# Performance work log

Hardware: AMD Instinct MI355X
Metric: run time of the kernel (lower is better)

Reference implementation:

```python
import jax, jax.numpy as jnp
import numpy as np
import math

MU = 0.1
NU = 10.0
UNITS = [512] * 8
FEATURES = 1024
BATCH = 8192
EPS = 1e-5


def _norm(x):
    return jnp.linalg.norm(x) + EPS


def _cayley(W):
    # Cayley orthogonalization; matches the torch reference (recursive transpose for wide matrices).
    cout, cin = W.shape
    if cin > cout:
        return _cayley(W.T).T
    U, V = W[:cin], W[cin:]
    I = jnp.eye(cin, dtype=W.dtype)
    A = U - U.T + V.T @ V
    iIpA = jnp.linalg.inv(I + A)
    return jnp.concatenate([iIpA @ (I - A), -2.0 * V @ iIpA], axis=0)


def setup_inputs() -> dict:
    key = jax.random.key(0)
    ks = jax.random.split(key, 5)
    sum_units = sum(UNITS)
    # xavier-normal-ish scales
    x = jax.random.normal(ks[0], (BATCH, FEATURES), jnp.float32)
    Fq = jax.random.normal(ks[1], (sum_units, FEATURES), jnp.float32) * math.sqrt(2.0 / (sum_units + FEATURES))
    fq = _norm(Fq).reshape(1)  # init.constant_(fq, norm(Fq))
    by = jnp.zeros((FEATURES,), jnp.float32)
    nz = UNITS[0]
    Fr0 = jax.random.normal(ks[2], (nz, nz), jnp.float32) * math.sqrt(2.0 / (nz + nz))
    Fr_rest = jax.random.normal(ks[3], (len(UNITS) - 1, nz, 2 * nz), jnp.float32) * math.sqrt(2.0 / (nz + 2 * nz))
    fr0 = _norm(Fr0).reshape(1)
    fr_rest = jnp.linalg.norm(Fr_rest, axis=(1, 2)) + EPS
    fr = jnp.concatenate([fr0, fr_rest])
    b = jnp.zeros((len(UNITS), nz), jnp.float32)
    return {"x": x, "Fq": Fq, "fq": fq, "by": by, "Fr0": Fr0, "Fr_rest": Fr_rest, "fr": fr, "b": b}


def reference(x, Fq, fq, by, Fr0, Fr_rest, fr, b):
    sqrt_gam = math.sqrt(NU - MU)
    sqrt2 = math.sqrt(2.0)
    # per-forward Cayley orthogonalization (training path)
    Q = _cayley(fq[0] * Fq / _norm(Fq))  # (sum_units, features)
    Rs = [_cayley(fr[0] * Fr0 / _norm(Fr0))]
    for k in range(Fr_rest.shape[0]):
        Rs.append(_cayley(fr[k + 1] * Fr_rest[k] / _norm(Fr_rest[k])))

    xh = sqrt_gam * (x @ Q.T)  # (B, sum_units)
    yh = []
    hk_1 = xh[..., :0]  # empty start
    idx = 0
    for k, nz in enumerate(UNITS):
        xk = xh[..., idx:idx + nz]
        pre = sqrt2 * (jnp.concatenate([xk, hk_1], axis=-1) @ Rs[k].T) + b[k]
        gh = sqrt2 * (jax.nn.relu(pre) @ Rs[k])  # (B, nz + nz_prev)
        hk = gh[..., :nz] - xk
        gk = gh[..., nz:]
        yh.append(hk_1 - gk)
        idx += nz
        hk_1 = hk
    yh.append(hk_1)
    yh = jnp.concatenate(yh, axis=-1)  # (B, sum_units)
    return 0.5 * ((MU + NU) * x + sqrt_gam * (yh @ Q)) + by
```

## Files before the change

### kernel.cpp

```cpp
#include <hip/hip_runtime.h>
#include <math.h>


using s8v = __attribute__((ext_vector_type(8))) short;
using f4v = __attribute__((ext_vector_type(4))) float;
typedef unsigned short ush;
typedef unsigned int uint32;

#define DEV __device__ __forceinline__

DEV float b2f(ush u){ union{unsigned int i; float f;} v; v.i = ((unsigned int)u)<<16; return v.f; }
DEV ush f2b(float f){
  union{float f; unsigned int i;} v; v.f = f;
  unsigned int u = v.i;
  return (ush)((u + 0x7fffu + ((u>>16)&1u)) >> 16);
}

typedef __attribute__((address_space(1))) void gvoid;
typedef __attribute__((address_space(3))) void lvoid;
DEV void gload16(const void* g, void* l){
  __builtin_amdgcn_global_load_lds((gvoid*)g, (lvoid*)l, 16, 0, 0);
}

DEV void st16(ush* dst, const ush* a){
  *(int4*)dst = *(const int4*)a; *(int4*)(dst+8) = *(const int4*)(a+8);
}

struct GA {
  const ush *A0h, *A0l; long lda0;
  const ush *A1h, *A1l; long lda1; int ksplit;
  const ush *Bh, *Bl; long ldb;
  int K, M, N;
  float alpha, beta;
  long sA, sB, sO, sD;
  void *o0,*o1,*o2,*o3,*o4;
  const void *e0,*e1;
  long ldo0, ldo1, ldE;
};

enum { E_F32=0, E_BF16=1, E_BF16T2=2, E_SPLIT=3, E_QW=4, E_PRE=5, E_GH=6, E_OUT=7 };

template<int BM, int BN, int EPI, bool SPLIT, bool TRX>
__global__ __launch_bounds__(256) void gemm_k(GA gq, GA gr, int zsplit)
{
  constexpr int AH = BM*32;
  constexpr int BH = BN*32;
  constexpr int PANEL = (AH+BH) * (SPLIT ? 2 : 1);
  constexpr int TBN = TRX ? 64*65*2 : 0;
  constexpr int SMN = (3*PANEL > TBN) ? 3*PANEL : TBN;
  __shared__ ush smem[SMN] __attribute__((aligned(16)));
  uint32* tb = (uint32*)smem;

  constexpr int LPS = (BM/64 + BN/64) * (SPLIT ? 2 : 1);

  GA g; int bz;
  if ((int)blockIdx.z < zsplit){ g = gq; bz = blockIdx.z; }
  else                         { g = gr; bz = blockIdx.z - zsplit; }

  const int gx = gridDim.x, gy = gridDim.y;
  const int lin = blockIdx.y*gx + blockIdx.x;
  const int per = gx*8;
  const int grp = lin / per;
  const int rem = lin - grp*per;
  int gh = gy - grp*8; if (gh > 8) gh = 8;
  const int by = grp*8 + rem % gh;
  const int bx = rem / gh;
  const int m0 = by * BM;
  const int n0 = bx * BN;
  if (m0 >= g.M || n0 >= g.N) return;

  const int t = threadIdx.x;
  const int lane = t & 63;
  const int wave = t >> 6;
  const int wm = (wave >> 1) * (BM/2);
  const int wn = (wave & 1) * (BN/2);
  constexpr int MT = BM/32;
  constexpr int NT = BN/32;

  const ush* Ah  = g.A0h + (long)bz*g.sA;
  const ush* Alp = SPLIT ? g.A0l + (long)bz*g.sA : nullptr;
  const ush* Bhp = g.Bh  + (long)bz*g.sB;
  const ush* Blp = SPLIT ? g.Bl  + (long)bz*g.sB : nullptr;

  f4v acc[MT][NT];
  #pragma unroll
  for (int i=0;i<MT;i++)
    #pragma unroll
    for (int j=0;j<NT;j++) acc[i][j] = f4v{0.f,0.f,0.f,0.f};

  const int sr  = lane >> 2;
  const int scg = lane & 3;

  auto STAGE = [&](int k0, int nb){
    ush* dA  = smem + nb*PANEL;
    ush* dB  = dA + AH;
    ush* dAl = dB + BH;
    ush* dBl = dAl + AH;
    #pragma unroll
    for (int p = 0; p < BM/64; ++p) {
      const int lr = wave*16 + sr + p*64;
      const int gc = scg ^ ((lr>>1)&3);
      const int kc = k0 + gc*8;
      long aoff; const ush* gp;
      if (kc < g.ksplit){ aoff = (long)(m0+lr)*g.lda0 + kc;               gp = Ah + aoff; }
      else              { aoff = (long)(m0+lr)*g.lda1 + (kc - g.ksplit);  gp = g.A1h + aoff; }
      gload16(gp, &dA[(wave*16 + p*64)*32]);
      if (SPLIT) gload16(Alp + aoff, &dAl[(wave*16 + p*64)*32]);
    }
    #pragma unroll
    for (int p = 0; p < BN/64; ++p) {
      const int lr = wave*16 + sr + p*64;
      const int gc = scg ^ ((lr>>1)&3);
      const long boff = (long)(n0+lr)*g.ldb + k0 + gc*8;
      gload16(Bhp + boff, &dB[(wave*16 + p*64)*32]);
      if (SPLIT) gload16(Blp + boff, &dBl[(wave*16 + p*64)*32]);
    }
  };

  STAGE(0, 0);
  int cur = 0;
  for (int k0 = 0; k0 < g.K; k0 += 32) {
    const int nxt = (cur==2) ? 0 : cur+1;
    if (k0 + 32 < g.K) {
      STAGE(k0 + 32, nxt);
      asm volatile("s_waitcnt vmcnt(%0)" :: "n"(LPS) : "memory");
    } else {
      asm volatile("s_waitcnt vmcnt(0)" ::: "memory");
    }
    __builtin_amdgcn_sched_barrier(0);
    __builtin_amdgcn_s_barrier();
    __builtin_amdgcn_sched_barrier(0);

    const ush* rA  = smem + cur*PANEL;
    const ush* rB  = rA + AH;
    const ush* rAl = rB + BH;
    const ush* rBl = rAl + AH;

    const int fr = lane & 15;
    const int cc = lane >> 4;
    s8v af[MT], bf_[NT];
    #pragma unroll
    for (int i=0;i<MT;i++){ const int row = wm + i*16 + fr;
      af[i] = *(const s8v*)(&rA[row*32 + ((cc ^ ((row>>1)&3))<<3)]); }
    #pragma unroll
    for (int j=0;j<NT;j++){ const int row = wn + j*16 + fr;
      bf_[j] = *(const s8v*)(&rB[row*32 + ((cc ^ ((row>>1)&3))<<3)]); }
    #pragma unroll
    for (int i=0;i<MT;i++)
      #pragma unroll
      for (int j=0;j<NT;j++)
        acc[i][j] = __builtin_amdgcn_mfma_f32_16x16x32_bf16(af[i], bf_[j], acc[i][j], 0,0,0);
    if (SPLIT) {
      s8v al2[MT], bl2[NT];
      #pragma unroll
      for (int j=0;j<NT;j++){ const int row = wn + j*16 + fr;
        bl2[j] = *(const s8v*)(&rBl[row*32 + ((cc ^ ((row>>1)&3))<<3)]); }
      #pragma unroll
      for (int i=0;i<MT;i++){ const int row = wm + i*16 + fr;
        al2[i] = *(const s8v*)(&rAl[row*32 + ((cc ^ ((row>>1)&3))<<3)]); }
      #pragma unroll
      for (int i=0;i<MT;i++)
        #pragma unroll
        for (int j=0;j<NT;j++)
          acc[i][j] = __builtin_amdgcn_mfma_f32_16x16x32_bf16(af[i], bl2[j], acc[i][j], 0,0,0);
      #pragma unroll
      for (int i=0;i<MT;i++)
        #pragma unroll
        for (int j=0;j<NT;j++)
          acc[i][j] = __builtin_amdgcn_mfma_f32_16x16x32_bf16(al2[i], bf_[j], acc[i][j], 0,0,0);
    }
    cur = nxt;
  }

  if constexpr (TRX) __syncthreads();

  #pragma unroll
  for (int i=0;i<MT;i++)
    #pragma unroll
    for (int j=0;j<NT;j++)
      #pragma unroll
      for (int r=0;r<4;r++) {
        const int lrow = wm + i*16 + ((lane>>4)<<2) + r;
        const int lcol = wn + j*16 + (lane & 15);
        const int grow = m0 + lrow;
        const int gcol = n0 + lcol;
        float v = g.alpha * acc[i][j][r];
        if constexpr (EPI == E_F32) {
          if (g.e0) v += g.beta * ((const float*)g.e0)[(long)bz*g.sD + (long)grow*g.ldo0 + gcol];
          ((float*)g.o0)[(long)bz*g.sO + (long)grow*g.ldo0 + gcol] = v;
        } else if constexpr (EPI == E_BF16) {
          if (g.e0) v += g.beta * b2f(((const ush*)g.e0)[(long)bz*g.sD + (long)grow*g.ldo0 + gcol]);
          ((ush*)g.o0)[(long)bz*g.sO + (long)grow*g.ldo0 + gcol] = f2b(v);
        } else if constexpr (EPI == E_BF16T2) {
          if (g.e0) v += g.beta * b2f(((const ush*)g.e0)[(long)bz*g.sD + (long)grow*g.ldo0 + gcol]);
          ush hv = f2b(v);
          ((ush*)g.o0)[(long)bz*g.sO + (long)grow*g.ldo0 + gcol] = hv;
          tb[lrow*65 + lcol] = hv;
        } else if constexpr (EPI == E_SPLIT) {
          if (g.e0) v += g.beta * ((const float*)g.e0)[(long)bz*g.sD + (long)grow*g.ldo0 + gcol];
          if (g.o0) ((float*)g.o0)[(long)bz*g.sO + (long)grow*g.ldo0 + gcol] = v;
          ush hv = f2b(v);
          ush lv = f2b(v - b2f(hv));
          ((ush*)g.o1)[(long)bz*g.sO + (long)grow*g.ldo0 + gcol] = hv;
          ((ush*)g.o2)[(long)bz*g.sO + (long)grow*g.ldo0 + gcol] = lv;
          if (TRX) tb[lrow*65 + lcol] = (uint32)hv | ((uint32)lv<<16);
        } else if constexpr (EPI == E_QW) {
          ush hv = f2b(v);
          ((ush*)g.o0)[(long)bz*g.sO + (long)grow*g.ldo0 + gcol] = hv;
          tb[lrow*65 + lcol] = hv;
        } else if constexpr (EPI == E_PRE) {
          v += ((const float*)g.e0)[gcol];
          v = v > 0.f ? v : 0.f;
          ((ush*)g.o0)[(long)grow*g.ldo0 + gcol] = f2b(v);
        } else if constexpr (EPI == E_GH) {
          if (gcol < 512) {
            float h = v - b2f(((const ush*)g.e0)[(long)grow*g.ldE + gcol]);
            ush hb = f2b(h);
            ((ush*)g.o0)[(long)grow*512 + gcol] = hb;
            if (g.o2) ((ush*)g.o2)[(long)grow*4096 + gcol] = hb;
          } else {
            float y = b2f(((const ush*)g.e1)[(long)grow*512 + (gcol-512)]) - v;
            ((ush*)g.o1)[(long)grow*4096 + (gcol-512)] = f2b(y);
          }
        } else if constexpr (EPI == E_OUT) {
          float o = 0.5f*(10.1f*((const float*)g.e0)[(long)grow*1024 + gcol] + v)
                  + ((const float*)g.e1)[gcol];
          ((float*)g.o0)[(long)grow*1024 + gcol] = o;
        }
      }

  if constexpr (TRX) {
    __syncthreads();
    const int tr  = t >> 2;
    const int seg = t & 3;
    uint32 vals[16];
    #pragma unroll
    for (int u=0;u<16;u++) vals[u] = tb[(seg*16+u)*65 + tr];
    ush hb[16] __attribute__((aligned(16)));
    ush lb[16] __attribute__((aligned(16)));
    #pragma unroll
    for (int u=0;u<16;u++){ hb[u] = (ush)(vals[u]&0xffffu); lb[u] = (ush)(vals[u]>>16); }
    const long bT = (long)bz*g.sO + (long)(n0+tr)*g.ldo1 + m0 + seg*16;
    if constexpr (EPI == E_BF16T2) {
      st16((ush*)g.o1 + bT, hb);
    } else if constexpr (EPI == E_SPLIT) {
      if (g.o3) { st16((ush*)g.o3 + bT, hb); st16((ush*)g.o4 + bT, lb); }
    } else if constexpr (EPI == E_QW) {
      st16((ush*)g.o1 + bT, hb);
    }
  }
}


__global__ __launch_bounds__(256) void k_norms(const float* __restrict__ Fq,
    const float* __restrict__ Fr0, const float* __restrict__ Frr, float* s2){
  const int y = blockIdx.y;
  const float* p; long cnt;
  if (y==0){ p=Fq; cnt=4194304l; }
  else if (y==1){ p=Fr0; cnt=262144l; }
  else { p=Frr + (long)(y-2)*524288; cnt=524288l; }
  float s = 0.f;
  for (long i = (long)blockIdx.x*256 + threadIdx.x; i < cnt; i += (long)gridDim.x*256){
    float v = p[i]; s += v*v;
  }
  #pragma unroll
  for (int o=32;o>0;o>>=1) s += __shfl_down(s, o, 64);
  __shared__ float red[4];
  if ((threadIdx.x & 63)==0) red[threadIdx.x>>6] = s;
  __syncthreads();
  if (threadIdx.x==0) atomicAdd(&s2[y], red[0]+red[1]+red[2]+red[3]);
}

__global__ void k_scales(const float* s2, const float* fq, const float* fr, float* sc){
  int t = threadIdx.x;
  if (t < 9){
    float v = (t==0)? fq[0] : fr[t-1];
    sc[t] = v / (sqrtf(s2[t]) + 1e-5f);
  }
}

__global__ __launch_bounds__(256) void k_buildT(const float* __restrict__ Fq,
    const float* __restrict__ Frr, const float* sc,
    ush* Vh, ush* Vl, ush* Vth, ush* Vtl,
    ush* Wrh, ush* Wrl, ush* WrTh, ush* WrTl){
  __shared__ uint32 tb[64*65];
  const int z = blockIdx.z;
  const int r = threadIdx.x >> 2;
  const int cs = (threadIdx.x & 3)*16;
  ush hh[16] __attribute__((aligned(16)));
  ush ll[16] __attribute__((aligned(16)));
  if (z==0){
    const long r0 = (long)blockIdx.y*64, c0 = (long)blockIdx.x*64;
    const float s = sc[0];
    const float* src = &Fq[(1024+r0+r)*1024 + c0 + cs];
    #pragma unroll
    for (int u=0;u<16;u++){
      float v = s*src[u];
      ush h = f2b(v); ush l = f2b(v - b2f(h));
      hh[u]=h; ll[u]=l;
      tb[r*65 + cs + u] = (uint32)h | ((uint32)l<<16);
    }
    st16(&Vh[(r0+r)*1024 + c0 + cs], hh);
    st16(&Vl[(r0+r)*1024 + c0 + cs], ll);
    __syncthreads();
    const int tr = threadIdx.x>>2, seg = threadIdx.x&3;
    #pragma unroll
    for (int u=0;u<16;u++){
      uint32 v = tb[(seg*16+u)*65 + tr];
      hh[u]=(ush)(v&0xffffu); ll[u]=(ush)(v>>16);
    }
    st16(&Vth[(c0+tr)*3072 + r0 + seg*16], hh);
    st16(&Vtl[(c0+tr)*3072 + r0 + seg*16], ll);
  } else {
    if (blockIdx.x>=8 || blockIdx.y>=8) return;
    const int k = z-1;
    const long r0 = (long)blockIdx.y*64, c0 = (long)blockIdx.x*64;
    const float s = sc[2+k];
    const float* src = &Frr[(long)k*524288 + (r0+r)*1024 + 512 + c0 + cs];
    #pragma unroll
    for (int u=0;u<16;u++){
      float v = s*src[u];
      ush h = f2b(v); ush l = f2b(v - b2f(h));
      hh[u]=h; ll[u]=l;
      tb[r*65 + cs + u] = (uint32)h | ((uint32)l<<16);
    }
    st16(&Wrh[(long)k*262144 + (r0+r)*512 + c0 + cs], hh);
    st16(&Wrl[(long)k*262144 + (r0+r)*512 + c0 + cs], ll);
    __syncthreads();
    const int tr = threadIdx.x>>2, seg = threadIdx.x&3;
    #pragma unroll
    for (int u=0;u<16;u++){
      uint32 v = tb[(seg*16+u)*65 + tr];
      hh[u]=(ush)(v&0xffffu); ll[u]=(ush)(v>>16);
    }
    st16(&WrTh[(long)k*262144 + (c0+tr)*512 + r0 + seg*16], hh);
    st16(&WrTl[(long)k*262144 + (c0+tr)*512 + r0 + seg*16], ll);
  }
}

__global__ __launch_bounds__(256) void k_asmT(const float* __restrict__ Fq,
    const float* __restrict__ Fr0, const float* __restrict__ Frr,
    const float* sc, const float* __restrict__ PP,
    ush* Mh, ush* Ml, ush* MTh, ush* MTl){
  __shared__ uint32 tb[64*65];
  const int z = blockIdx.z;
  const int r = threadIdx.x >> 2;
  const int cs = (threadIdx.x & 3)*16;
  const long ROFF = 1048576l, RS = 262144l;
  long r0 = (long)blockIdx.y*64, c0 = (long)blockIdx.x*64;
  const float* dsrc; const float* msrc; const float* psrc = nullptr;
  float s; long obase; long old_; float sgn;
  if (z==0){
    s = sc[0]; sgn = 1.f;
    dsrc = &Fq[(r0+r)*1024 + c0 + cs];
    msrc = &Fq[(c0+r)*1024 + r0 + cs];
    psrc = &PP[(r0+r)*1024 + c0 + cs];
    obase = 0; old_ = 1024;
  } else {
    if (blockIdx.x>=8 || blockIdx.y>=8) return;
    const int b = z-1;
    if (b==0){
      s = sc[1]; sgn = 1.f;
      dsrc = &Fr0[(r0+r)*512 + c0 + cs];
      msrc = &Fr0[(c0+r)*512 + r0 + cs];
    } else {
      s = sc[1+b]; sgn = -1.f;
      const float* W = Frr + (long)(b-1)*524288;
      dsrc = &W[(r0+r)*1024 + c0 + cs];
      msrc = &W[(c0+r)*1024 + r0 + cs];
      psrc = &PP[ROFF + (long)(b-1)*RS + (r0+r)*512 + c0 + cs];
    }
    obase = ROFF + (long)b*RS; old_ = 512;
  }
  #pragma unroll
  for (int u=0;u<16;u++) tb[r*65 + cs + u] = __float_as_uint(msrc[u]);
  __syncthreads();
  ush hh[16] __attribute__((aligned(16)));
  ush ll[16] __attribute__((aligned(16)));
  #pragma unroll
  for (int u=0;u<16;u++){
    const int c = cs + u;
    float mir = __uint_as_float(tb[c*65 + r]);
    float a = sgn * s * (dsrc[u] - mir);
    if (psrc) a += psrc[u];
    float m = ((r0 + r == c0 + c) ? 1.f : 0.f) + a;
    ush h = f2b(m); ush l = f2b(m - b2f(h));
    hh[u]=h; ll[u]=l;
  }
  st16(&Mh[obase + (r0+r)*old_ + c0 + cs], hh);
  st16(&Ml[obase + (r0+r)*old_ + c0 + cs], ll);
  __syncthreads();
  #pragma unroll
  for (int u=0;u<16;u++) tb[r*65 + cs + u] = (uint32)hh[u] | ((uint32)ll[u]<<16);
  __syncthreads();
  const int tr = threadIdx.x>>2, seg = threadIdx.x&3;
  #pragma unroll
  for (int u=0;u<16;u++){
    uint32 v = tb[(seg*16+u)*65 + tr];
    hh[u]=(ush)(v&0xffffu); ll[u]=(ush)(v>>16);
  }
  st16(&MTh[obase + (c0+tr)*old_ + r0 + seg*16], hh);
  st16(&MTl[obase + (c0+tr)*old_ + r0 + seg*16], ll);
}

__global__ __launch_bounds__(256) void k_rowabs(const float* __restrict__ T2, float* bmax){
  const int y = blockIdx.y;
  const float* row; int n;
  if (y==0){ row = T2 + (long)blockIdx.x*1024; n = 1024; }
  else { if (blockIdx.x >= 512) return;
         row = T2 + 1048576l + (long)(y-1)*262144 + (long)blockIdx.x*512; n = 512; }
  float s=0.f;
  for (int i=threadIdx.x;i<n;i+=256) s += fabsf(row[i]);
  #pragma unroll
  for (int o=32;o>0;o>>=1) s += __shfl_down(s,o,64);
  __shared__ float red[4];
  if ((threadIdx.x&63)==0) red[threadIdx.x>>6]=s;
  __syncthreads();
  if (threadIdx.x==0){
    float tot = red[0]+red[1]+red[2]+red[3];
    atomicMax((unsigned int*)&bmax[y], __float_as_uint(tot));
  }
}

__global__ void k_makec(const float* bmax, float* cvl){
  int t=threadIdx.x;
  if (t<9){
    float bnd = sqrtf(fmaxf(bmax[t], 1.f));
    cvl[t] = 1.9f/(1.f + bnd);
  }
}

__global__ __launch_bounds__(256) void k_initX(const ush* __restrict__ Mh,
    const ush* __restrict__ MTh, const float* cvl, ush* Xh, ush* XTh){
  long i = (long)blockIdx.x*256 + threadIdx.x;
  int b = (i < 1048576l) ? 0 : 1 + (int)((i - 1048576l) >> 18);
  float c = cvl[b];
  Xh[i]  = f2b(c * b2f(MTh[i]));
  XTh[i] = f2b(c * b2f(Mh[i]));
}

__global__ __launch_bounds__(256) void k_promote(const ush* __restrict__ Xh,
    float* Xf, ush* Xl, ush* XTl){
  long i = (long)blockIdx.x*256 + threadIdx.x;
  Xf[i] = b2f(Xh[i]);
  Xl[i] = 0; XTl[i] = 0;
}

__global__ __launch_bounds__(256) void k_topT(const ush* __restrict__ Xh, const ush* __restrict__ Xl,
    ush* Qb, ush* QTb, ush* RK, ush* RKT){
  __shared__ uint32 tb[64*65];
  const int z = blockIdx.z;
  const int r = threadIdx.x >> 2;
  const int cs = (threadIdx.x & 3)*16;
  const long ROFF = 1048576l, RS = 262144l;
  long r0 = (long)blockIdx.y*64, c0 = (long)blockIdx.x*64;
  ush hh[16] __attribute__((aligned(16)));
  if (z==0){
    const long base = (r0+r)*1024 + c0 + cs;
    #pragma unroll
    for (int u=0;u<16;u++){
      float v = 2.f*(b2f(Xh[base+u]) + b2f(Xl[base+u])) - ((r0+r == c0+cs+u)?1.f:0.f);
      hh[u] = f2b(v);
      tb[r*65 + cs + u] = hh[u];
    }
    st16(&Qb[(r0+r)*1024 + c0 + cs], hh);
    __syncthreads();
    const int tr = threadIdx.x>>2, seg = threadIdx.x&3;
    #pragma unroll
    for (int u=0;u<16;u++) hh[u] = (ush)tb[(seg*16+u)*65 + tr];
    st16(&QTb[(c0+tr)*4096 + r0 + seg*16], hh);
  } else {
    if (blockIdx.x>=8 || blockIdx.y>=8) return;
    const int b = z-1;
    const long base = ROFF + (long)b*RS + (r0+r)*512 + c0 + cs;
    #pragma unroll
    for (int u=0;u<16;u++){
      float v = 2.f*(b2f(Xh[base+u]) + b2f(Xl[base+u])) - ((r0+r == c0+cs+u)?1.f:0.f);
      hh[u] = f2b(v);
      tb[r*65 + cs + u] = hh[u];
    }
    st16(&RKT[(long)b*524288 + (r0+r)*512 + c0 + cs], hh);
    __syncthreads();
    const int tr = threadIdx.x>>2, seg = threadIdx.x&3;
    #pragma unroll
    for (int u=0;u<16;u++) hh[u] = (ush)tb[(seg*16+u)*65 + tr];
    st16(&RK[(long)b*524288 + (c0+tr)*1024 + r0 + seg*16], hh);
  }
}

__global__ __launch_bounds__(256) void k_f2bf(const float* __restrict__ in, ush* __restrict__ o){
  long i = ((long)blockIdx.x*256 + threadIdx.x)*8;
  float4 a = *(const float4*)(in+i);
  float4 b = *(const float4*)(in+i+4);
  ush u[8] __attribute__((aligned(16)));
  u[0]=f2b(a.x);u[1]=f2b(a.y);u[2]=f2b(a.z);u[3]=f2b(a.w);
  u[4]=f2b(b.x);u[5]=f2b(b.y);u[6]=f2b(b.z);u[7]=f2b(b.w);
  *(int4*)(o+i) = *(const int4*)u;
}


static GA mk(const ush* Ah, const ush* Al, long lda,
             const ush* Bh, const ush* Bl, long ldb,
             int K, int M, int N, float alpha){
  GA g{}; g.ksplit=1<<30; g.A0h=Ah; g.A0l=Al; g.lda0=lda;
  g.Bh=Bh; g.Bl=Bl; g.ldb=ldb; g.K=K; g.M=M; g.N=N; g.alpha=alpha; g.beta=0.f;
  return g;
}

extern "C" void kernel_launch(void* const* d_in, const int* in_sizes, int n_in,
                              void* d_out, int out_size, void* d_ws, size_t ws_size,
                              hipStream_t stream)
{
  (void)in_sizes; (void)n_in; (void)out_size; (void)ws_size;
  const float* x   = (const float*)d_in[0];
  const float* Fq  = (const float*)d_in[1];
  const float* fqp = (const float*)d_in[2];
  const float* by  = (const float*)d_in[3];
  const float* Fr0 = (const float*)d_in[4];
  const float* Frr = (const float*)d_in[5];
  const float* frp = (const float*)d_in[6];
  const float* bp  = (const float*)d_in[7];
  float* out = (float*)d_out;

  const float SQG = sqrtf(10.0f - 0.1f);
  const float SQ2 = sqrtf(2.0f);
  const long UN = 3145728l;
  const long ROFF = 1048576l, RS = 262144l;

  char* base = (char*)d_ws;
  size_t off = 0;
  auto alloc = [&](size_t bytes)->char*{
    char* p = base + off; off = (off + bytes + 255) & ~(size_t)255; return p;
  };

  ush* Qb  = (ush*)alloc(4194304l*2);
  ush* QTb = (ush*)alloc(4194304l*2);
  ush* RK  = (ush*)alloc(4194304l*2);
  ush* RKT = (ush*)alloc(4194304l*2);
  ush* xbf = (ush*)alloc(8388608l*2);
  float* scal = (float*)alloc(256*4);
  float* s2   = scal;
  float* bmax = scal + 16;
  float* cvl  = scal + 32;
  float* sc   = scal + 48;

  const size_t scratch0 = off;
  ush* Vh   = (ush*)alloc(UN*2);
  ush* Vl   = (ush*)alloc(UN*2);
  ush* Vth  = (ush*)alloc(UN*2);
  ush* Vtl  = (ush*)alloc(UN*2);
  ush* Wrh  = (ush*)alloc(1835008l*2);
  ush* Wrl  = (ush*)alloc(1835008l*2);
  ush* WrTh = (ush*)alloc(1835008l*2);
  ush* WrTl = (ush*)alloc(1835008l*2);
  float* PPf = (float*)alloc(UN*4);
  ush* Mh  = (ush*)alloc(UN*2);
  ush* Ml  = (ush*)alloc(UN*2);
  ush* MTh = (ush*)alloc(UN*2);
  ush* MTl = (ush*)alloc(UN*2);
  ush* Sh  = (ush*)alloc(UN*2);
  ush* XhA = (ush*)alloc(UN*2);
  ush* XhB = (ush*)alloc(UN*2);
  ush* XlA = (ush*)alloc(UN*2);
  ush* XlB = (ush*)alloc(UN*2);
  ush* XThA = (ush*)alloc(UN*2);
  ush* XThB = (ush*)alloc(UN*2);
  ush* XTlA = (ush*)alloc(UN*2);
  ush* XTlB = (ush*)alloc(UN*2);
  float* XfA = (float*)alloc(UN*4);
  float* XfB = (float*)alloc(UN*4);
  ush* Yh  = (ush*)alloc(UN*2);
  ush* Yl  = (ush*)alloc(UN*2);

  ush* Xh[2]  = {XhA, XhB};
  ush* Xl[2]  = {XlA, XlB};
  ush* XTh[2] = {XThA, XThB};
  ush* XTl[2] = {XTlA, XTlB};
  float* Xf[2] = {XfA, XfB};

  dim3 B256(256);
  GA ga{}, gr{};

  (void)hipMemsetAsync(scal, 0, 1024, stream);
  k_norms<<<dim3(64,9),B256,0,stream>>>(Fq, Fr0, Frr, s2);
  k_scales<<<1,16,0,stream>>>(s2, fqp, frp, sc);

  k_buildT<<<dim3(16,48,8),B256,0,stream>>>(Fq, Frr, sc, Vh,Vl,Vth,Vtl, Wrh,Wrl,WrTh,WrTl);

  ga = mk(Vth,Vtl,3072, Vth,Vtl,3072, 3072,1024,1024, 1.f); ga.o0=PPf; ga.ldo0=1024;
  gr = mk(Wrh,Wrl,512, Wrh,Wrl,512, 512,512,512, 1.f);
  gr.sA=RS; gr.sB=RS; gr.o0=PPf+ROFF; gr.sO=RS; gr.ldo0=512;
  gemm_k<64,64,E_F32,true,false><<<dim3(16,16,8),B256,0,stream>>>(ga,gr,1);

  k_asmT<<<dim3(16,16,9),B256,0,stream>>>(Fq, Fr0, Frr, sc, PPf, Mh,Ml,MTh,MTl);

  ga = mk(Mh,nullptr,1024, Mh,nullptr,1024, 1024,1024,1024, 1.f); ga.o0=Sh; ga.ldo0=1024;
  gr = mk(Mh+ROFF,nullptr,512, Mh+ROFF,nullptr,512, 512,512,512, 1.f);
  gr.sA=RS; gr.sB=RS; gr.o0=Sh+ROFF; gr.sO=RS; gr.ldo0=512;
  gemm_k<64,64,E_BF16,false,false><<<dim3(16,16,9),B256,0,stream>>>(ga,gr,1);

  ga = mk(Sh,nullptr,1024, Sh,nullptr,1024, 1024,1024,1024, 1.f); ga.o0=PPf; ga.ldo0=1024;
  gr = mk(Sh+ROFF,nullptr,512, Sh+ROFF,nullptr,512, 512,512,512, 1.f);
  gr.sA=RS; gr.sB=RS; gr.o0=PPf+ROFF; gr.sO=RS; gr.ldo0=512;
  gemm_k<64,64,E_F32,false,false><<<dim3(16,16,9),B256,0,stream>>>(ga,gr,1);
  k_rowabs<<<dim3(1024,9),B256,0,stream>>>(PPf, bmax);
  k_makec<<<1,16,0,stream>>>(bmax, cvl);
  k_initX<<<12288,B256,0,stream>>>(Mh, MTh, cvl, Xh[0], XTh[0]);

  int cur = 0;
  for (int it=0; it<9; ++it){
    int nxt = cur^1;
    ga = mk(XTh[cur],nullptr,1024, Mh,nullptr,1024, 1024,1024,1024, 1.f); ga.o0=Yh; ga.ldo0=1024;
    gr = mk(XTh[cur]+ROFF,nullptr,512, Mh+ROFF,nullptr,512, 512,512,512, 1.f);
    gr.sA=RS; gr.sB=RS; gr.o0=Yh+ROFF; gr.sO=RS; gr.ldo0=512;
    gemm_k<64,64,E_BF16,false,false><<<dim3(16,16,9),B256,0,stream>>>(ga,gr,1);

    ga = mk(Xh[cur],nullptr,1024, Yh,nullptr,1024, 1024,1024,1024, -1.f);
    ga.beta=2.f; ga.e0=Xh[cur];
    ga.o0=Xh[nxt]; ga.o1=XTh[nxt]; ga.ldo0=1024; ga.ldo1=1024;
    gr = mk(Xh[cur]+ROFF,nullptr,512, Yh+ROFF,nullptr,512, 512,512,512, -1.f);
    gr.beta=2.f; gr.e0=Xh[cur]+ROFF; gr.sD=RS;
    gr.sA=RS; gr.sB=RS; gr.sO=RS;
    gr.o0=Xh[nxt]+ROFF; gr.o1=XTh[nxt]+ROFF; gr.ldo0=512; gr.ldo1=512;
    gemm_k<64,64,E_BF16T2,false,true><<<dim3(16,16,9),B256,0,stream>>>(ga,gr,1);
    cur = nxt;
  }

  k_promote<<<12288,B256,0,stream>>>(Xh[cur], Xf[cur], Xl[cur], XTl[cur]);
  for (int it=0; it<2; ++it){
    int nxt = cur^1;
    ga = mk(XTh[cur],XTl[cur],1024, Mh,Ml,1024, 1024,1024,1024, 1.f);
    ga.o1=Yh; ga.o2=Yl; ga.ldo0=1024;
    gr = mk(XTh[cur]+ROFF,XTl[cur]+ROFF,512, Mh+ROFF,Ml+ROFF,512, 512,512,512, 1.f);
    gr.sA=RS; gr.sB=RS; gr.o1=Yh+ROFF; gr.o2=Yl+ROFF; gr.sO=RS; gr.ldo0=512;
    gemm_k<64,64,E_SPLIT,true,false><<<dim3(16,16,9),B256,0,stream>>>(ga,gr,1);

    ga = mk(Xh[cur],Xl[cur],1024, Yh,Yl,1024, 1024,1024,1024, -1.f);
    ga.beta=2.f; ga.e0=Xf[cur];
    ga.o0=Xf[nxt]; ga.o1=Xh[nxt]; ga.o2=Xl[nxt]; ga.o3=XTh[nxt]; ga.o4=XTl[nxt];
    ga.ldo0=1024; ga.ldo1=1024;
    gr = mk(Xh[cur]+ROFF,Xl[cur]+ROFF,512, Yh+ROFF,Yl+ROFF,512, 512,512,512, -1.f);
    gr.beta=2.f; gr.e0=Xf[cur]+ROFF; gr.sD=RS;
    gr.sA=RS; gr.sB=RS; gr.sO=RS;
    gr.o0=Xf[nxt]+ROFF; gr.o1=Xh[nxt]+ROFF; gr.o2=Xl[nxt]+ROFF;
    gr.o3=XTh[nxt]+ROFF; gr.o4=XTl[nxt]+ROFF;
    gr.ldo0=512; gr.ldo1=512;
    gemm_k<64,64,E_SPLIT,true,true><<<dim3(16,16,9),B256,0,stream>>>(ga,gr,1);
    cur = nxt;
  }

  k_topT<<<dim3(16,16,9),B256,0,stream>>>(Xh[cur], Xl[cur], Qb, QTb, RK, RKT);

  ga = mk(Vh,Vl,1024, XTh[cur],XTl[cur],1024, 1024,3072,1024, -2.f);
  ga.o0=Qb + 1048576l; ga.ldo0=1024; ga.o1=QTb + 1024; ga.ldo1=4096;
  gr = mk(WrTh,WrTl,512, XTh[cur]+ROFF+RS, XTl[cur]+ROFF+RS, 512, 512,512,512, -2.f);
  gr.sA=RS; gr.sB=RS; gr.sO=524288;
  gr.o0=RKT + 524288 + 262144; gr.ldo0=512;
  gr.o1=RK + 524288 + 512; gr.ldo1=1024;
  gemm_k<64,64,E_QW,true,true><<<dim3(16,48,8),B256,0,stream>>>(ga,gr,1);

  off = scratch0;
  ush* xh  = (ush*)alloc(33554432l*2);
  ush* yh  = (ush*)alloc(33554432l*2);
  ush* pre = (ush*)alloc(4194304l*2);
  ush* h0  = (ush*)alloc(4194304l*2);
  ush* h1  = (ush*)alloc(4194304l*2);

  k_f2bf<<<4096,B256,0,stream>>>(x, xbf);
  ga = mk(xbf,nullptr,1024, Qb,nullptr,1024, 1024,8192,4096, SQG);
  ga.o0=xh; ga.ldo0=4096;
  gemm_k<128,128,E_BF16,false,false><<<dim3(32,64,1),B256,0,stream>>>(ga,ga,1);

  for (int k=0;k<8;++k){
    ush* hprev = (k==0)? nullptr : (((k-1)&1) ? h1 : h0);
    ush* hnew  = (k&1) ? h1 : h0;
    GA gp_ = mk(xh + (long)k*512, nullptr, 4096,
                (k==0)? RKT : RK + (long)k*524288, nullptr, (k==0)?512:1024,
                (k==0)?512:1024, 8192, 512, SQ2);
    gp_.ksplit = 512; gp_.A1h = hprev; gp_.lda1 = 512;
    gp_.e0 = bp + (long)k*512; gp_.o0 = pre; gp_.ldo0 = 512;
    gemm_k<128,64,E_PRE,false,false><<<dim3(8,64,1),B256,0,stream>>>(gp_,gp_,1);

    GA gg = mk(pre, nullptr, 512,
               (k==0)? RK : RKT + (long)k*524288, nullptr, (k==0)?1024:512,
               512, 8192, (k==0)?512:1024, SQ2);
    gg.e0 = xh + (long)k*512; gg.ldE = 4096;
    gg.e1 = hprev;
    gg.o0 = hnew;
    gg.o1 = (k>=1)? (void*)(yh + (long)(k-1)*512) : nullptr;
    gg.o2 = (k==7)? (void*)(yh + 3584) : nullptr;
    if (k==0) gemm_k<128,64,E_GH,false,false><<<dim3(8,64,1),B256,0,stream>>>(gg,gg,1);
    else      gemm_k<128,128,E_GH,false,false><<<dim3(8,64,1),B256,0,stream>>>(gg,gg,1);
  }

  ga = mk(yh,nullptr,4096, QTb,nullptr,4096, 4096,8192,1024, SQG);
  ga.e0=x; ga.e1=by; ga.o0=out; ga.ldo0=1024;
  gemm_k<128,128,E_OUT,false,false><<<dim3(8,64,1),B256,0,stream>>>(ga,ga,1);
}
```

Baseline: 1.527 ms.

## Deepen GEMM prefetch to two stages and vectorize norm reduction

The GEMM main loop now prefetches two K-slices ahead (four LDS buffers) when the panel is small enough, and waits on the older group of loads with a wider vmcnt, so more global-to-LDS traffic is in flight while MFMAs run. Larger split panels keep the single-stage prefetch. Separately, the Frobenius-norm kernel reads float4 and uses more blocks to raise memory throughput. The deeper pipeline costs extra shared memory, which can reduce occupancy.

Result: faster. 1.464 ms (-4.1%).

```diff
diff --git a/kernel.cpp b/kernel.cpp
--- a/kernel.cpp
+++ b/kernel.cpp
@@ -46,8 +46,10 @@
   constexpr int AH = BM*32;
   constexpr int BH = BN*32;
   constexpr int PANEL = (AH+BH) * (SPLIT ? 2 : 1);
+  constexpr int DEPTH = (PANEL <= 6144) ? 2 : 1;
+  constexpr int NBUF  = DEPTH + 2;
   constexpr int TBN = TRX ? 64*65*2 : 0;
-  constexpr int SMN = (3*PANEL > TBN) ? 3*PANEL : TBN;
+  constexpr int SMN = (NBUF*PANEL > TBN) ? NBUF*PANEL : TBN;
   __shared__ ush smem[SMN] __attribute__((aligned(16)));
   uint32* tb = (uint32*)smem;
 
@@ -118,14 +120,28 @@
   };
 
   STAGE(0, 0);
+  if (DEPTH == 2 && g.K > 32) STAGE(32, 1);
   int cur = 0;
   for (int k0 = 0; k0 < g.K; k0 += 32) {
-    const int nxt = (cur==2) ? 0 : cur+1;
-    if (k0 + 32 < g.K) {
-      STAGE(k0 + 32, nxt);
-      asm volatile("s_waitcnt vmcnt(%0)" :: "n"(LPS) : "memory");
+    const int rem_steps = ((g.K - k0) >> 5) - 1;
+    if (DEPTH == 2) {
+      if (rem_steps >= 2) {
+        const int nb = (cur+2 >= NBUF) ? cur+2-NBUF : cur+2;
+        STAGE(k0 + 64, nb);
+        asm volatile("s_waitcnt vmcnt(%0)" :: "n"(2*LPS) : "memory");
+      } else if (rem_steps == 1) {
+        asm volatile("s_waitcnt vmcnt(%0)" :: "n"(LPS) : "memory");
+      } else {
+        asm volatile("s_waitcnt vmcnt(0)" ::: "memory");
+      }
     } else {
-      asm volatile("s_waitcnt vmcnt(0)" ::: "memory");
+      if (rem_steps >= 1) {
+        const int nb = (cur+1 >= NBUF) ? cur+1-NBUF : cur+1;
+        STAGE(k0 + 32, nb);
+        asm volatile("s_waitcnt vmcnt(%0)" :: "n"(LPS) : "memory");
+      } else {
+        asm volatile("s_waitcnt vmcnt(0)" ::: "memory");
+      }
     }
     __builtin_amdgcn_sched_barrier(0);
     __builtin_amdgcn_s_barrier();
@@ -169,7 +185,7 @@
         for (int j=0;j<NT;j++)
           acc[i][j] = __builtin_amdgcn_mfma_f32_16x16x32_bf16(al2[i], bf_[j], acc[i][j], 0,0,0);
     }
-    cur = nxt;
+    cur = (cur+1 >= NBUF) ? 0 : cur+1;
   }
 
   if constexpr (TRX) __syncthreads();
@@ -255,13 +271,14 @@
 __global__ __launch_bounds__(256) void k_norms(const float* __restrict__ Fq,
     const float* __restrict__ Fr0, const float* __restrict__ Frr, float* s2){
   const int y = blockIdx.y;
-  const float* p; long cnt;
-  if (y==0){ p=Fq; cnt=4194304l; }
-  else if (y==1){ p=Fr0; cnt=262144l; }
-  else { p=Frr + (long)(y-2)*524288; cnt=524288l; }
+  const float* p; long cnt4;
+  if (y==0){ p=Fq; cnt4=1048576l; }
+  else if (y==1){ p=Fr0; cnt4=65536l; }
+  else { p=Frr + (long)(y-2)*524288; cnt4=131072l; }
   float s = 0.f;
-  for (long i = (long)blockIdx.x*256 + threadIdx.x; i < cnt; i += (long)gridDim.x*256){
-    float v = p[i]; s += v*v;
+  for (long i = (long)blockIdx.x*256 + threadIdx.x; i < cnt4; i += (long)gridDim.x*256){
+    float4 v = ((const float4*)p)[i];
+    s += v.x*v.x + v.y*v.y + v.z*v.z + v.w*v.w;
   }
   #pragma unroll
   for (int o=32;o>0;o>>=1) s += __shfl_down(s, o, 64);
@@ -582,7 +599,7 @@
   GA ga{}, gr{};
 
   (void)hipMemsetAsync(scal, 0, 1024, stream);
-  k_norms<<<dim3(64,9),B256,0,stream>>>(Fq, Fr0, Frr, s2);
+  k_norms<<<dim3(256,9),B256,0,stream>>>(Fq, Fr0, Frr, s2);
   k_scales<<<1,16,0,stream>>>(s2, fqp, frp, sc);
 
   k_buildT<<<dim3(16,48,8),B256,0,stream>>>(Fq, Frr, sc, Vh,Vl,Vth,Vtl, Wrh,Wrl,WrTh,WrTl);
```
